# Performance work log

Measured on AMD Instinct MI355X. Metric: run time of the kernel, lower is better.

The kernel has to match this reference:

```python
import jax, jax.numpy as jnp
import numpy as np

B, T, N = 64, 128, 64   # batch, win_size, input_size (= node_num)
H, E, K, CS = 64, 128, 7, 8  # hidden_size, embed_size, kernel_size, control_size
NEG_SLOPE = 0.2


def _p(key, shape, scale=0.05):
    return scale * jax.random.normal(key, shape, dtype=jnp.float32)


def setup_inputs() -> dict:
    key = jax.random.key(0)
    ks = jax.random.split(key, 32)
    inp = {
        "x": jax.random.normal(ks[0], (B, T, N), dtype=jnp.float32),
        "y": jax.random.normal(ks[1], (B, T, CS), dtype=jnp.float32),
        # Conv1d(N -> N, kernel K)
        "conv_w": _p(ks[2], (N, N, K)),
        "conv_b": _p(ks[3], (N,)),
        # rnn_enc GRU: input N -> hidden H
        "We_ih": _p(ks[4], (3 * H, N)), "We_hh": _p(ks[5], (3 * H, H)),
        "be_ih": _p(ks[6], (3 * H,)), "be_hh": _p(ks[7], (3 * H,)),
        # MP_GAT linears
        "Ww": _p(ks[8], (E, 2 * T)), "bw": _p(ks[9], (E,)),
        "Wa": _p(ks[10], (1, E)), "ba": _p(ks[11], (1,)),
        # encoder GRU: input H+N -> H
        "Wm_ih": _p(ks[12], (3 * H, H + N)), "Wm_hh": _p(ks[13], (3 * H, H)),
        "bm_ih": _p(ks[14], (3 * H,)), "bm_hh": _p(ks[15], (3 * H,)),
        # rnn_dec GRU: input H -> H
        "Wd_ih": _p(ks[16], (3 * H, H)), "Wd_hh": _p(ks[17], (3 * H, H)),
        "bd_ih": _p(ks[18], (3 * H,)), "bd_hh": _p(ks[19], (3 * H,)),
        # fc_dec: H -> N
        "W_dec": _p(ks[20], (N, H)), "b_dec": _p(ks[21], (N,)),
        # fc_pred: Linear(H,N), ReLU, Linear(N,N)
        "W_p1": _p(ks[22], (N, H)), "b_p1": _p(ks[23], (N,)),
        "W_p2": _p(ks[24], (N, N)), "b_p2": _p(ks[25], (N,)),
    }
    return inp


def gru_seq(x_seq, Wih, Whh, bih, bhh):
    """torch nn.GRU (batch_first, h0=0). x_seq: [B,T,in] -> [B,T,H]."""
    gi = jnp.einsum('bti,gi->btg', x_seq, Wih) + bih  # [B,T,3H] (precompute input proj)
    h0 = jnp.zeros((x_seq.shape[0], Whh.shape[1]), x_seq.dtype)

    def step(h, gi_t):
        gh = h @ Whh.T + bhh
        i_r, i_z, i_n = jnp.split(gi_t, 3, axis=-1)
        h_r, h_z, h_n = jnp.split(gh, 3, axis=-1)
        r = jax.nn.sigmoid(i_r + h_r)
        z = jax.nn.sigmoid(i_z + h_z)
        n = jnp.tanh(i_n + r * h_n)
        h_new = (1.0 - z) * n + z * h
        return h_new, h_new

    _, hs = jax.lax.scan(step, h0, jnp.swapaxes(gi, 0, 1))
    return jnp.swapaxes(hs, 0, 1)


def _forward(x, y, conv_w, conv_b, We_ih, We_hh, be_ih, be_hh, Ww, bw, Wa, ba,
             Wm_ih, Wm_hh, bm_ih, bm_hh, Wd_ih, Wd_hh, bd_ih, bd_hh,
             W_dec, b_dec, W_p1, b_p1, W_p2, b_p2):
    # ---- CNN: pad 'same' + Conv1d + SELU. x: [B,T,N] -> channels first [B,N,T]
    pad = (K - 1) // 2
    xc = jnp.swapaxes(x, 1, 2)
    c = jax.lax.conv_general_dilated(xc, conv_w, (1,), [(pad, pad)],
                                     dimension_numbers=('NCH', 'OIH', 'NCH'))
    c = jax.nn.selu(c + conv_b[None, :, None])  # [B,N,T]
    c_btn = jnp.swapaxes(c, 1, 2)               # [B,T,N]

    # ---- rnn_enc GRU over time
    h_out = gru_seq(c_btn, We_ih, We_hh, be_ih, be_hh)  # [B,T,H]

    # ---- MP_GAT on c (v: [B, node, seq] = [B,N,T])
    v = c
    vi = jnp.broadcast_to(v[:, :, None, :], (B, N, N, T))
    vj = jnp.broadcast_to(v[:, None, :, :], (B, N, N, T))
    v_cat = jnp.concatenate([vi, vj], axis=-1)          # [B,N,N,2T]
    x_w = jax.nn.leaky_relu(jnp.einsum('bijt,et->bije', v_cat, Ww) + bw, NEG_SLOPE)
    e = (jnp.einsum('bije,oe->bijo', x_w, Wa) + ba)[..., 0]  # [B,N,N]
    attention = jax.nn.softmax(e, axis=2)
    # dropout is identity in eval mode
    h_mp = jax.nn.sigmoid(jnp.einsum('bij,bjt->bit', attention, v))  # [B,N,T]
    h_mp = jnp.swapaxes(h_mp, 1, 2)                      # [B,T,N]

    # ---- encoder / decoder GRUs (dropout = identity in eval)
    h_cat = jnp.concatenate([h_out, h_mp], axis=2)       # [B,T,H+N]
    h_enc = gru_seq(h_cat, Wm_ih, Wm_hh, bm_ih, bm_hh)
    h_dec = gru_seq(h_enc, Wd_ih, Wd_hh, bd_ih, bd_hh)

    recon = h_dec @ W_dec.T + b_dec                      # [B,T,N]
    p = jax.nn.relu(h_dec[:, 0, :] @ W_p1.T + b_p1)
    pred = p @ W_p2.T + b_p2                             # [B,N]
    return recon, pred


def reference(x, y, conv_w, conv_b, We_ih, We_hh, be_ih, be_hh, Ww, bw, Wa, ba,
              Wm_ih, Wm_hh, bm_ih, bm_hh, Wd_ih, Wd_hh, bd_ih, bd_hh,
              W_dec, b_dec, W_p1, b_p1, W_p2, b_p2):
    return _forward(x, y, conv_w, conv_b, We_ih, We_hh, be_ih, be_hh, Ww, bw, Wa, ba,
                    Wm_ih, Wm_hh, bm_ih, bm_hh, Wd_ih, Wd_hh, bd_ih, bd_hh,
                    W_dec, b_dec, W_p1, b_p1, W_p2, b_p2)
```

## Files before the change

### kernel.cpp

```cpp
#include <hip/hip_runtime.h>
#include <math.h>

#define BB 64
#define TT 128
#define NN 64
#define HH 64
#define EE 128
#define KK 7
#define GG 192

typedef _Float16 half2_t __attribute__((ext_vector_type(2)));

__device__ __forceinline__ float sigmoidf_(float x){ return 1.f/(1.f+expf(-x)); }
__device__ __forceinline__ float fsig_(float x){
  return __builtin_amdgcn_rcpf(1.f + __builtin_amdgcn_exp2f(-1.44269504f * x));
}
__device__ __forceinline__ float ftanh_(float x){
  return fmaf(-2.f, __builtin_amdgcn_rcpf(1.f + __builtin_amdgcn_exp2f(2.88539008f * x)), 1.f);
}

#define PIPE_BARRIER() asm volatile("s_waitcnt lgkmcnt(0)\ns_barrier" ::: "memory")
#define LGKM0() asm volatile("s_waitcnt lgkmcnt(0)" ::: "memory")

__device__ __forceinline__ void loadrow_(float* d, const float* src){
  const float4* p = (const float4*)src;
  #pragma unroll
  for (int i = 0; i < 16; ++i) {
    float4 v = p[i];
    d[4*i] = v.x; d[4*i+1] = v.y; d[4*i+2] = v.z; d[4*i+3] = v.w;
  }
}
__device__ __forceinline__ void loadroww_(half2_t* d, const float* src){
  const float4* p = (const float4*)src;
  #pragma unroll
  for (int i = 0; i < 16; ++i) {
    float4 v = p[i];
    d[2*i]   = half2_t{(_Float16)v.x, (_Float16)v.y};
    d[2*i+1] = half2_t{(_Float16)v.z, (_Float16)v.w};
  }
}
__device__ __forceinline__ void load_h16_(const _Float16* hs, half2_t* hp){
  const float4* s4 = (const float4*)hs;
  #pragma unroll
  for (int j = 0; j < 8; ++j) {
    float4 v = s4[j];
    const half2_t* q = (const half2_t*)&v;
    hp[4*j] = q[0]; hp[4*j+1] = q[1]; hp[4*j+2] = q[2]; hp[4*j+3] = q[3];
  }
}
__device__ __forceinline__ void mvdot3_(const half2_t* hp, const half2_t* w0,
                                        const half2_t* w1, const half2_t* w2,
                                        float& a0, float& a1, float& a2){
  #pragma unroll
  for (int i = 0; i < 32; ++i) {
    a0 = __builtin_amdgcn_fdot2(hp[i], w0[i], a0, false);
    a1 = __builtin_amdgcn_fdot2(hp[i], w1[i], a1, false);
    a2 = __builtin_amdgcn_fdot2(hp[i], w2[i], a2, false);
  }
}

__global__ void conv_s12_kernel(const float* __restrict__ x, const float* __restrict__ w,
                                const float* __restrict__ bias, const float* __restrict__ Ww,
                                float* __restrict__ c_nt, float* __restrict__ c_btn,
                                float* __restrict__ s1, float* __restrict__ s2) {
  const int og = blockIdx.x, b = blockIdx.y, t = threadIdx.x;
  const int o0 = og * 8;
  __shared__ __align__(16) float xs[NN][TT + 1];
  __shared__ __align__(16) float ws[NN * KK][8];
  __shared__ __align__(16) float cs[8][TT];
  for (int idx = t; idx < TT * NN; idx += 128) {
    int tt = idx >> 6, nn = idx & 63;
    xs[nn][tt] = x[(size_t)(b * TT + tt) * NN + nn];
  }
  for (int idx = t; idx < NN * KK * 8; idx += 128) {
    int oo = idx & 7, ik = idx >> 3;
    ws[ik][oo] = w[(size_t)(o0 + oo) * (NN * KK) + ik];
  }
  __syncthreads();
  float acc[8];
  #pragma unroll
  for (int oo = 0; oo < 8; ++oo) acc[oo] = bias[o0 + oo];
  for (int i = 0; i < NN; ++i) {
    #pragma unroll
    for (int k = 0; k < KK; ++k) {
      int tt = t + k - 3;
      if (tt >= 0 && tt < TT) {
        float xv = xs[i][tt];
        const float* wp = &ws[i * KK + k][0];
        float4 w0 = *(const float4*)wp;
        float4 w1 = *(const float4*)(wp + 4);
        acc[0] += xv * w0.x; acc[1] += xv * w0.y; acc[2] += xv * w0.z; acc[3] += xv * w0.w;
        acc[4] += xv * w1.x; acc[5] += xv * w1.y; acc[6] += xv * w1.z; acc[7] += xv * w1.w;
      }
    }
  }
  const float alpha = 1.6732632423543772f, scale = 1.0507009873554805f;
  #pragma unroll
  for (int oo = 0; oo < 8; ++oo) {
    float a = acc[oo];
    float r = a > 0.f ? scale * a : scale * alpha * expm1f(a);
    int o = o0 + oo;
    c_nt[((size_t)b * NN + o) * TT + t] = r;
    c_btn[((size_t)b * TT + t) * NN + o] = r;
    cs[oo][t] = r;
  }
  __syncthreads();
  const float* w1 = Ww + (size_t)t * (2 * TT);
  const float* w2 = w1 + TT;
  float a1[8], a2l[8];
  #pragma unroll
  for (int r = 0; r < 8; ++r) { a1[r] = 0.f; a2l[r] = 0.f; }
  #pragma unroll 2
  for (int k = 0; k < TT; k += 4) {
    float4 wv1 = *(const float4*)(w1 + k);
    float4 wv2 = *(const float4*)(w2 + k);
    #pragma unroll
    for (int r = 0; r < 8; ++r) {
      float4 cv = *(const float4*)&cs[r][k];
      a1[r]  += cv.x * wv1.x + cv.y * wv1.y + cv.z * wv1.z + cv.w * wv1.w;
      a2l[r] += cv.x * wv2.x + cv.y * wv2.y + cv.z * wv2.z + cv.w * wv2.w;
    }
  }
  #pragma unroll
  for (int r = 0; r < 8; ++r) {
    s1[((size_t)b * NN + o0 + r) * EE + t] = a1[r];
    s2[((size_t)b * NN + o0 + r) * EE + t] = a2l[r];
  }
}

__global__ void gat_kernel(const float* __restrict__ s1, const float* __restrict__ s2,
                           const float* __restrict__ bw, const float* __restrict__ Wa,
                           const float* __restrict__ ba, const float* __restrict__ c_nt,
                           float* __restrict__ hmp) {
  const int it = blockIdx.x, b = blockIdx.y, tid = threadIdx.x;
  const int i0 = it * 16;
  __shared__ float s2s[NN][EE + 1];
  __shared__ float s1b[16][EE];
  __shared__ float cs[NN][TT + 1];
  __shared__ float was[EE];
  __shared__ float att[16][NN];
  for (int idx = tid; idx < NN * EE; idx += 256) {
    int j = idx >> 7, e = idx & 127;
    s2s[j][e] = s2[((size_t)b * NN + j) * EE + e] + bw[e];
  }
  for (int idx = tid; idx < 16 * EE; idx += 256) {
    int r = idx >> 7, e = idx & 127;
    s1b[r][e] = s1[((size_t)b * NN + i0 + r) * EE + e];
  }
  for (int idx = tid; idx < NN * TT; idx += 256) {
    int j = idx >> 7, t = idx & 127;
    cs[j][t] = c_nt[((size_t)b * NN + j) * TT + t];
  }
  if (tid < EE) was[tid] = Wa[tid];
  __syncthreads();
  const int wv = tid >> 6, j = tid & 63;
  #pragma unroll
  for (int pass = 0; pass < 4; ++pass) {
    const int il = pass * 4 + wv;
    float acc = 0.f;
    #pragma unroll 8
    for (int e = 0; e < EE; ++e) {
      float v = s1b[il][e] + s2s[j][e];
      v = v > 0.f ? v : 0.2f * v;
      acc += was[e] * v;
    }
    float ej = acc + ba[0];
    float mx = ej;
    for (int off = 32; off >= 1; off >>= 1) mx = fmaxf(mx, __shfl_xor(mx, off));
    float ex = __builtin_amdgcn_exp2f(1.44269504f * (ej - mx));
    float sm = ex;
    for (int off = 32; off >= 1; off >>= 1) sm += __shfl_xor(sm, off);
    att[il][j] = ex / sm;
  }
  __syncthreads();
  for (int o = tid; o < 16 * TT; o += 256) {
    int il = o >> 7, t = o & 127;
    float acc = 0.f;
    #pragma unroll 8
    for (int jj = 0; jj < NN; ++jj) acc += att[il][jj] * cs[jj][t];
    hmp[((size_t)b * TT + t) * NN + i0 + il] = sigmoidf_(acc);
  }
}

__global__ __launch_bounds__(512, 1)
void fused_chain8(const float* __restrict__ c_btn, const float* __restrict__ hmp,
                  const float* __restrict__ We_ih, const float* __restrict__ be_ih,
                  const float* __restrict__ We_hh, const float* __restrict__ be_hh,
                  const float* __restrict__ Wm_ih, const float* __restrict__ bm_ih,
                  const float* __restrict__ Wm_hh, const float* __restrict__ bm_hh,
                  const float* __restrict__ Wd_ih, const float* __restrict__ bd_ih,
                  const float* __restrict__ Wd_hh, const float* __restrict__ bd_hh,
                  const float* __restrict__ W_dec, const float* __restrict__ b_dec,
                  const float* __restrict__ W_p1, const float* __restrict__ b_p1,
                  const float* __restrict__ W_p2, const float* __restrict__ b_p2,
                  float* __restrict__ recon, float* __restrict__ pred) {
  const int b = blockIdx.x, tid = threadIdx.x, wid = tid >> 6, g = tid & 63;
  __shared__ __align__(16) _Float16 cbuf[2][HH], mbuf[2][HH];
  __shared__ __align__(16) _Float16 h1h[2][HH], h2h[2][HH], h3h[2][HH];
  __shared__ __align__(16) float h3f[2][HH];
  __shared__ __align__(16) float q1[2][GG], q2a[2][GG], q2b[2][GG], q3[2][GG];
  __shared__ __align__(16) float h0s[HH], ps[HH];

  half2_t wa[32], wb[32], wc[32];
  float wdec[64];
  float b0 = 0.f, b1 = 0.f, b2 = 0.f;
  float e0 = 0.f, e1 = 0.f, e2 = 0.f;
  if (wid == 0) {
    loadroww_(wa, We_hh + (size_t)g * HH);
    loadroww_(wb, We_hh + (size_t)(g + 64) * HH);
    loadroww_(wc, We_hh + (size_t)(g + 128) * HH);
    b0 = be_hh[g]; b1 = be_hh[64 + g]; b2 = be_hh[128 + g];
  } else if (wid == 1) {
    loadroww_(wa, Wm_hh + (size_t)g * HH);
    loadroww_(wb, Wm_hh + (size_t)(g + 64) * HH);
    loadroww_(wc, Wm_hh + (size_t)(g + 128) * HH);
    b0 = bm_hh[g]; b1 = bm_hh[64 + g]; b2 = bm_hh[128 + g];
  } else if (wid == 2) {
    loadroww_(wa, Wd_hh + (size_t)g * HH);
    loadroww_(wb, Wd_hh + (size_t)(g + 64) * HH);
    loadroww_(wc, Wd_hh + (size_t)(g + 128) * HH);
    b0 = bd_hh[g]; b1 = bd_hh[64 + g]; b2 = bd_hh[128 + g];
    e0 = bd_ih[g]; e1 = bd_ih[64 + g]; e2 = bd_ih[128 + g];
  } else if (wid == 3) {
    loadrow_(wdec, W_dec + (size_t)g * HH);
    b0 = b_dec[g];
  } else if (wid == 4) {
    loadroww_(wa, Wm_ih + (size_t)g * 128);
    loadroww_(wb, Wm_ih + (size_t)(g + 64) * 128);
    loadroww_(wc, Wm_ih + (size_t)(g + 128) * 128);
  } else if (wid == 5) {
    loadroww_(wa, Wd_ih + (size_t)g * HH);
    loadroww_(wb, Wd_ih + (size_t)(g + 64) * HH);
    loadroww_(wc, Wd_ih + (size_t)(g + 128) * HH);
  } else if (wid == 6) {
    loadroww_(wa, We_ih + (size_t)g * HH);
    loadroww_(wb, We_ih + (size_t)(g + 64) * HH);
    loadroww_(wc, We_ih + (size_t)(g + 128) * HH);
    b0 = be_ih[g]; b1 = be_ih[64 + g]; b2 = be_ih[128 + g];
  } else {
    loadroww_(wa, Wm_ih + (size_t)g * 128 + 64);
    loadroww_(wb, Wm_ih + (size_t)(g + 64) * 128 + 64);
    loadroww_(wc, Wm_ih + (size_t)(g + 128) * 128 + 64);
    b0 = bm_ih[g]; b1 = bm_ih[64 + g]; b2 = bm_ih[128 + g];
  }

  if (wid == 0) {
    h1h[0][g] = (_Float16)0.f; h1h[1][g] = (_Float16)0.f;
    h2h[0][g] = (_Float16)0.f; h2h[1][g] = (_Float16)0.f;
    h3h[0][g] = (_Float16)0.f; h3h[1][g] = (_Float16)0.f;
  }
  const float* cb = c_btn + (size_t)b * TT * NN + g;
  const float* hm = hmp   + (size_t)b * TT * NN + g;
  float pf0 = 0.f, pf1 = 0.f;
  if (wid == 6) {
    cbuf[0][g] = (_Float16)cb[0]; cbuf[1][g] = (_Float16)cb[NN];
    pf0 = cb[2 * NN]; pf1 = cb[3 * NN];
  }
  if (wid == 7) {
    mbuf[0][g] = (_Float16)hm[0]; mbuf[1][g] = (_Float16)hm[NN];
    pf0 = hm[2 * NN]; pf1 = hm[3 * NN];
  }
  if (wid <= 2) __builtin_amdgcn_s_setprio(1);
  __syncthreads();

  float hown = 0.f;
  for (int ph = 0; ph < TT + 6; ++ph) {
    const int pw = ph & 1, pr = pw ^ 1;
    if (wid == 6) {
      int t = ph;
      if (t < TT) {
        half2_t hp[32]; load_h16_(&cbuf[pw][0], hp);
        if (t + 2 < TT) cbuf[pw][g] = (_Float16)(pw ? pf1 : pf0);
        float a0 = b0, a1 = b1, a2 = b2;
        if (t + 4 < TT) { float nv = cb[(size_t)(t + 4) * NN]; if (pw) pf1 = nv; else pf0 = nv; }
        mvdot3_(hp, wa, wb, wc, a0, a1, a2);
        q1[pw][g] = a0; q1[pw][64 + g] = a1; q1[pw][128 + g] = a2;
      }
    } else if (wid == 0) {
      int t = ph - 1;
      if (t >= 0 && t < TT) {
        half2_t hp[32]; load_h16_(&h1h[pr][0], hp);
        float a0 = b0, a1 = b1, a2 = b2;
        mvdot3_(hp, wa, wb, wc, a0, a1, a2);
        float r = fsig_(q1[pr][g] + a0), z = fsig_(q1[pr][64 + g] + a1);
        float n = ftanh_(q1[pr][128 + g] + r * a2);
        hown = fmaf(z, hown - n, n);
        h1h[pw][g] = (_Float16)hown;
      }
    } else if (wid == 4) {
      int t = ph - 2;
      if (t >= 0 && t < TT) {
        half2_t hp[32]; load_h16_(&h1h[pr][0], hp);
        float a0 = 0.f, a1 = 0.f, a2 = 0.f;
        mvdot3_(hp, wa, wb, wc, a0, a1, a2);
        q2a[pw][g] = a0; q2a[pw][64 + g] = a1; q2a[pw][128 + g] = a2;
      }
    } else if (wid == 7) {
      int t = ph - 2;
      if (t >= 0 && t < TT) {
        half2_t hp[32]; load_h16_(&mbuf[pw][0], hp);
        if (t + 2 < TT) mbuf[pw][g] = (_Float16)(pw ? pf1 : pf0);
        float a0 = b0, a1 = b1, a2 = b2;
        if (t + 4 < TT) { float nv = hm[(size_t)(t + 4) * NN]; if (pw) pf1 = nv; else pf0 = nv; }
        mvdot3_(hp, wa, wb, wc, a0, a1, a2);
        q2b[pw][g] = a0; q2b[pw][64 + g] = a1; q2b[pw][128 + g] = a2;
      }
    } else if (wid == 1) {
      int t = ph - 3;
      if (t >= 0 && t < TT) {
        half2_t hp[32]; load_h16_(&h2h[pr][0], hp);
        float a0 = b0, a1 = b1, a2 = b2;
        mvdot3_(hp, wa, wb, wc, a0, a1, a2);
        float gr = q2a[pr][g] + q2b[pr][g];
        float gz = q2a[pr][64 + g] + q2b[pr][64 + g];
        float gn = q2a[pr][128 + g] + q2b[pr][128 + g];
        float r = fsig_(gr + a0), z = fsig_(gz + a1), n = ftanh_(gn + r * a2);
        hown = fmaf(z, hown - n, n);
        h2h[pw][g] = (_Float16)hown;
      }
    } else if (wid == 5) {
      int t = ph - 4;
      if (t >= 0 && t < TT) {
        half2_t hp[32]; load_h16_(&h2h[pr][0], hp);
        float a0 = 0.f, a1 = 0.f, a2 = 0.f;
        mvdot3_(hp, wa, wb, wc, a0, a1, a2);
        q3[pw][g] = a0; q3[pw][64 + g] = a1; q3[pw][128 + g] = a2;
      }
    } else if (wid == 2) {
      int t = ph - 5;
      if (t >= 0 && t < TT) {
        half2_t hp[32]; load_h16_(&h3h[pr][0], hp);
        float a0 = b0, a1 = b1, a2 = b2;
        mvdot3_(hp, wa, wb, wc, a0, a1, a2);
        float r = fsig_(q3[pr][g] + e0 + a0), z = fsig_(q3[pr][64 + g] + e1 + a1);
        float n = ftanh_(q3[pr][128 + g] + e2 + r * a2);
        hown = fmaf(z, hown - n, n);
        h3h[pw][g] = (_Float16)hown;
        h3f[pw][g] = hown;
        if (t == 0) h0s[g] = hown;
      }
    } else {
      int t = ph - 6;
      if (t >= 0) {
        const float4* h4 = (const float4*)&h3f[pr][0];
        float a0 = b0, a1 = 0.f;
        #pragma unroll
        for (int i = 0; i < 8; ++i) {
          float4 hv = h4[2 * i], hw = h4[2 * i + 1];
          a0 = fmaf(hv.x, wdec[8*i],   fmaf(hv.y, wdec[8*i+1], fmaf(hv.z, wdec[8*i+2], fmaf(hv.w, wdec[8*i+3], a0))));
          a1 = fmaf(hw.x, wdec[8*i+4], fmaf(hw.y, wdec[8*i+5], fmaf(hw.z, wdec[8*i+6], fmaf(hw.w, wdec[8*i+7], a1))));
        }
        recon[((size_t)b * TT + t) * NN + g] = a0 + a1;
      }
    }
    PIPE_BARRIER();
  }

  if (wid == 0) {
    float w1r[64]; loadrow_(w1r, W_p1 + (size_t)g * HH);
    const float4* h4 = (const float4*)&h0s[0];
    float a = b_p1[g];
    #pragma unroll
    for (int i = 0; i < 16; ++i) {
      float4 hv = h4[i];
      a = fmaf(hv.x, w1r[4*i], fmaf(hv.y, w1r[4*i+1], fmaf(hv.z, w1r[4*i+2], fmaf(hv.w, w1r[4*i+3], a))));
    }
    ps[g] = fmaxf(a, 0.f);
    LGKM0();
    float w2r[64]; loadrow_(w2r, W_p2 + (size_t)g * HH);
    const float4* p4 = (const float4*)&ps[0];
    float c2 = b_p2[g];
    #pragma unroll
    for (int i = 0; i < 16; ++i) {
      float4 pv = p4[i];
      c2 = fmaf(pv.x, w2r[4*i], fmaf(pv.y, w2r[4*i+1], fmaf(pv.z, w2r[4*i+2], fmaf(pv.w, w2r[4*i+3], c2))));
    }
    pred[(size_t)b * NN + g] = c2;
  }
}

extern "C" void kernel_launch(void* const* d_in, const int* in_sizes, int n_in,
                              void* d_out, int out_size, void* d_ws, size_t ws_size,
                              hipStream_t stream) {
  const float* x      = (const float*)d_in[0];
  const float* conv_w = (const float*)d_in[2];
  const float* conv_b = (const float*)d_in[3];
  const float* We_ih  = (const float*)d_in[4];
  const float* We_hh  = (const float*)d_in[5];
  const float* be_ih  = (const float*)d_in[6];
  const float* be_hh  = (const float*)d_in[7];
  const float* Ww     = (const float*)d_in[8];
  const float* bw     = (const float*)d_in[9];
  const float* Wa     = (const float*)d_in[10];
  const float* ba     = (const float*)d_in[11];
  const float* Wm_ih  = (const float*)d_in[12];
  const float* Wm_hh  = (const float*)d_in[13];
  const float* bm_ih  = (const float*)d_in[14];
  const float* bm_hh  = (const float*)d_in[15];
  const float* Wd_ih  = (const float*)d_in[16];
  const float* Wd_hh  = (const float*)d_in[17];
  const float* bd_ih  = (const float*)d_in[18];
  const float* bd_hh  = (const float*)d_in[19];
  const float* W_dec  = (const float*)d_in[20];
  const float* b_dec  = (const float*)d_in[21];
  const float* W_p1   = (const float*)d_in[22];
  const float* b_p1   = (const float*)d_in[23];
  const float* W_p2   = (const float*)d_in[24];
  const float* b_p2   = (const float*)d_in[25];
  float* out = (float*)d_out;

  float* wsf   = (float*)d_ws;
  float* c_nt  = wsf;
  float* c_btn = c_nt  + 524288;
  float* s1    = c_btn + 524288;
  float* s2    = s1    + 524288;
  float* hmp   = s2    + 524288;

  conv_s12_kernel<<<dim3(8, BB), 128, 0, stream>>>(x, conv_w, conv_b, Ww,
                                                   c_nt, c_btn, s1, s2);
  gat_kernel<<<dim3(4, BB), 256, 0, stream>>>(s1, s2, bw, Wa, ba, c_nt, hmp);
  fused_chain8<<<BB, 512, 0, stream>>>(c_btn, hmp,
                                       We_ih, be_ih, We_hh, be_hh,
                                       Wm_ih, bm_ih, Wm_hh, bm_hh,
                                       Wd_ih, bd_ih, Wd_hh, bd_hh,
                                       W_dec, b_dec, W_p1, b_p1, W_p2, b_p2,
                                       out, out + BB * TT * NN);
}
```

Baseline: 182.6 us.

## Fuse GAT attention into recurrent chain kernel with swizzled fp16 LDS buffer

```diff
diff --git a/kernel.cpp b/kernel.cpp
--- a/kernel.cpp
+++ b/kernel.cpp
@@ -128,78 +128,79 @@
   }
 }
 
-__global__ void gat_kernel(const float* __restrict__ s1, const float* __restrict__ s2,
-                           const float* __restrict__ bw, const float* __restrict__ Wa,
-                           const float* __restrict__ ba, const float* __restrict__ c_nt,
-                           float* __restrict__ hmp) {
-  const int it = blockIdx.x, b = blockIdx.y, tid = threadIdx.x;
-  const int i0 = it * 16;
-  __shared__ float s2s[NN][EE + 1];
-  __shared__ float s1b[16][EE];
-  __shared__ float cs[NN][TT + 1];
-  __shared__ float was[EE];
-  __shared__ float att[16][NN];
-  for (int idx = tid; idx < NN * EE; idx += 256) {
+__global__ __launch_bounds__(512, 1)
+void gat_chain8(const float* __restrict__ s1, const float* __restrict__ s2,
+                const float* __restrict__ bw, const float* __restrict__ Wa,
+                const float* __restrict__ ba, const float* __restrict__ c_nt,
+                const float* __restrict__ c_btn,
+                const float* __restrict__ We_ih, const float* __restrict__ be_ih,
+                const float* __restrict__ We_hh, const float* __restrict__ be_hh,
+                const float* __restrict__ Wm_ih, const float* __restrict__ bm_ih,
+                const float* __restrict__ Wm_hh, const float* __restrict__ bm_hh,
+                const float* __restrict__ Wd_ih, const float* __restrict__ bd_ih,
+                const float* __restrict__ Wd_hh, const float* __restrict__ bd_hh,
+                const float* __restrict__ W_dec, const float* __restrict__ b_dec,
+                const float* __restrict__ W_p1, const float* __restrict__ b_p1,
+                const float* __restrict__ W_p2, const float* __restrict__ b_p2,
+                float* __restrict__ recon, float* __restrict__ pred) {
+  const int b = blockIdx.x, tid = threadIdx.x, wid = tid >> 6, g = tid & 63;
+  __shared__ __align__(16) float s2s[NN][EE + 1];
+  __shared__ __align__(16) float s1b[NN][EE];
+  __shared__ __align__(16) float csn[NN][TT + 4];
+  __shared__ __align__(16) float attb[NN][NN];
+  __shared__ __align__(16) float wasl[EE];
+  __shared__ __align__(16) _Float16 hmph[TT][NN];
+  __shared__ __align__(16) _Float16 cbuf[2][HH];
+  __shared__ __align__(16) _Float16 h1h[2][HH], h2h[2][HH], h3h[2][HH];
+  __shared__ __align__(16) float h3f[2][HH];
+  __shared__ __align__(16) float q1[2][GG], q2a[2][GG], q2b[2][GG], q3[2][GG];
+  __shared__ __align__(16) float h0s[HH], ps[HH];
+
+  for (int idx = tid; idx < NN * EE; idx += 512) {
     int j = idx >> 7, e = idx & 127;
     s2s[j][e] = s2[((size_t)b * NN + j) * EE + e] + bw[e];
   }
-  for (int idx = tid; idx < 16 * EE; idx += 256) {
-    int r = idx >> 7, e = idx & 127;
-    s1b[r][e] = s1[((size_t)b * NN + i0 + r) * EE + e];
-  }
-  for (int idx = tid; idx < NN * TT; idx += 256) {
-    int j = idx >> 7, t = idx & 127;
-    cs[j][t] = c_nt[((size_t)b * NN + j) * TT + t];
-  }
-  if (tid < EE) was[tid] = Wa[tid];
+  for (int idx = tid; idx < NN * EE; idx += 512) {
+    int j = idx >> 7, e = idx & 127;
+    s1b[j][e] = s1[((size_t)b * NN + j) * EE + e];
+  }
+  for (int idx = tid; idx < NN * TT; idx += 512) {
+    int n = idx >> 7, t = idx & 127;
+    csn[n][t] = c_nt[((size_t)b * NN + n) * TT + t];
+  }
+  if (tid < EE) wasl[tid] = Wa[tid];
   __syncthreads();
-  const int wv = tid >> 6, j = tid & 63;
-  #pragma unroll
-  for (int pass = 0; pass < 4; ++pass) {
-    const int il = pass * 4 + wv;
+
+  const float ba0 = ba[0];
+  #pragma unroll
+  for (int pass = 0; pass < 8; ++pass) {
+    const int i = pass * 8 + wid;
     float acc = 0.f;
     #pragma unroll 8
     for (int e = 0; e < EE; ++e) {
-      float v = s1b[il][e] + s2s[j][e];
+      float v = s1b[i][e] + s2s[g][e];
       v = v > 0.f ? v : 0.2f * v;
-      acc += was[e] * v;
-    }
-    float ej = acc + ba[0];
+      acc += wasl[e] * v;
+    }
+    float ej = acc + ba0;
     float mx = ej;
     for (int off = 32; off >= 1; off >>= 1) mx = fmaxf(mx, __shfl_xor(mx, off));
     float ex = __builtin_amdgcn_exp2f(1.44269504f * (ej - mx));
     float sm = ex;
     for (int off = 32; off >= 1; off >>= 1) sm += __shfl_xor(sm, off);
-    att[il][j] = ex / sm;
+    attb[i][g] = ex / sm;
   }
   __syncthreads();
-  for (int o = tid; o < 16 * TT; o += 256) {
-    int il = o >> 7, t = o & 127;
+
+  for (int it = tid; it < NN * TT; it += 512) {
+    const int i = it >> 7, t = it & 127;
     float acc = 0.f;
     #pragma unroll 8
-    for (int jj = 0; jj < NN; ++jj) acc += att[il][jj] * cs[jj][t];
-    hmp[((size_t)b * TT + t) * NN + i0 + il] = sigmoidf_(acc);
-  }
-}
-
-__global__ __launch_bounds__(512, 1)
-void fused_chain8(const float* __restrict__ c_btn, const float* __restrict__ hmp,
-                  const float* __restrict__ We_ih, const float* __restrict__ be_ih,
-                  const float* __restrict__ We_hh, const float* __restrict__ be_hh,
-                  const float* __restrict__ Wm_ih, const float* __restrict__ bm_ih,
-                  const float* __restrict__ Wm_hh, const float* __restrict__ bm_hh,
-                  const float* __restrict__ Wd_ih, const float* __restrict__ bd_ih,
-                  const float* __restrict__ Wd_hh, const float* __restrict__ bd_hh,
-                  const float* __restrict__ W_dec, const float* __restrict__ b_dec,
-                  const float* __restrict__ W_p1, const float* __restrict__ b_p1,
-                  const float* __restrict__ W_p2, const float* __restrict__ b_p2,
-                  float* __restrict__ recon, float* __restrict__ pred) {
-  const int b = blockIdx.x, tid = threadIdx.x, wid = tid >> 6, g = tid & 63;
-  __shared__ __align__(16) _Float16 cbuf[2][HH], mbuf[2][HH];
-  __shared__ __align__(16) _Float16 h1h[2][HH], h2h[2][HH], h3h[2][HH];
-  __shared__ __align__(16) float h3f[2][HH];
-  __shared__ __align__(16) float q1[2][GG], q2a[2][GG], q2b[2][GG], q3[2][GG];
-  __shared__ __align__(16) float h0s[HH], ps[HH];
+    for (int j = 0; j < NN; ++j) acc += attb[i][j] * csn[j][t];
+    float hv = sigmoidf_(acc);
+    int iphys = (i & 7) | ((((i >> 3) ^ (t & 7)) & 7) << 3);
+    hmph[t][iphys] = (_Float16)hv;
+  }
 
   half2_t wa[32], wb[32], wc[32];
   float wdec[64];
@@ -250,15 +251,10 @@
     h3h[0][g] = (_Float16)0.f; h3h[1][g] = (_Float16)0.f;
   }
   const float* cb = c_btn + (size_t)b * TT * NN + g;
-  const float* hm = hmp   + (size_t)b * TT * NN + g;
   float pf0 = 0.f, pf1 = 0.f;
   if (wid == 6) {
     cbuf[0][g] = (_Float16)cb[0]; cbuf[1][g] = (_Float16)cb[NN];
     pf0 = cb[2 * NN]; pf1 = cb[3 * NN];
-  }
-  if (wid == 7) {
-    mbuf[0][g] = (_Float16)hm[0]; mbuf[1][g] = (_Float16)hm[NN];
-    pf0 = hm[2 * NN]; pf1 = hm[3 * NN];
   }
   if (wid <= 2) __builtin_amdgcn_s_setprio(1);
   __syncthreads();
@@ -298,10 +294,16 @@
     } else if (wid == 7) {
       int t = ph - 2;
       if (t >= 0 && t < TT) {
-        half2_t hp[32]; load_h16_(&mbuf[pw][0], hp);
-        if (t + 2 < TT) mbuf[pw][g] = (_Float16)(pw ? pf1 : pf0);
+        half2_t hp[32];
+        const int sw = t & 7;
+        const float4* s4 = (const float4*)&hmph[t][0];
+        #pragma unroll
+        for (int j = 0; j < 8; ++j) {
+          float4 v = s4[j ^ sw];
+          const half2_t* q = (const half2_t*)&v;
+          hp[4*j] = q[0]; hp[4*j+1] = q[1]; hp[4*j+2] = q[2]; hp[4*j+3] = q[3];
+        }
         float a0 = b0, a1 = b1, a2 = b2;
-        if (t + 4 < TT) { float nv = hm[(size_t)(t + 4) * NN]; if (pw) pf1 = nv; else pf0 = nv; }
         mvdot3_(hp, wa, wb, wc, a0, a1, a2);
         q2b[pw][g] = a0; q2b[pw][64 + g] = a1; q2b[pw][128 + g] = a2;
       }
@@ -414,15 +416,13 @@
   float* c_btn = c_nt  + 524288;
   float* s1    = c_btn + 524288;
   float* s2    = s1    + 524288;
-  float* hmp   = s2    + 524288;
 
   conv_s12_kernel<<<dim3(8, BB), 128, 0, stream>>>(x, conv_w, conv_b, Ww,
                                                    c_nt, c_btn, s1, s2);
-  gat_kernel<<<dim3(4, BB), 256, 0, stream>>>(s1, s2, bw, Wa, ba, c_nt, hmp);
-  fused_chain8<<<BB, 512, 0, stream>>>(c_btn, hmp,
-                                       We_ih, be_ih, We_hh, be_hh,
-                                       Wm_ih, bm_ih, Wm_hh, bm_hh,
-                                       Wd_ih, bd_ih, Wd_hh, bd_hh,
-                                       W_dec, b_dec, W_p1, b_p1, W_p2, b_p2,
-                                       out, out + BB * TT * NN);
-}
+  gat_chain8<<<BB, 512, 0, stream>>>(s1, s2, bw, Wa, ba, c_nt, c_btn,
+                                     We_ih, be_ih, We_hh, be_hh,
+                                     Wm_ih, bm_ih, Wm_hh, bm_hh,
+                                     Wd_ih, bd_ih, Wd_hh, bd_hh,
+                                     W_dec, b_dec, W_p1, b_p1, W_p2, b_p2,
+                                     out, out + BB * TT * NN);
+}
```

Measured after the change: 203.7 us. 1.12x slower.
